# Kernel optimization log

Hardware: AMD Instinct MI355X
Metric: run time of the kernel (lower is better)

## Reference

```python
import jax, jax.numpy as jnp
import numpy as np

B, DIM, DQ, H, W, K = 64, 64, 8, 64, 64, 64


def setup_inputs() -> dict:
    key = jax.random.key(0)
    k1, k2, k3 = jax.random.split(key, 3)
    features = jax.random.normal(k1, (B, DIM, H, W), dtype=jnp.float32)
    query = jax.random.normal(k2, (B, DQ, H, W), dtype=jnp.float32)
    # Ensemble of K 1x1 convs (Conv2d(dim, dim_query, 1, bias=False)) -> [K, DQ, DIM]
    weight = jax.random.normal(k3, (K, DQ, DIM), dtype=jnp.float32) * (1.0 / np.sqrt(DIM))
    return {"features": features, "query": query, "weight": weight}


def reference(features, query, weight):
    # Ensemble of K 1x1 convs: key_values [k, b, dq, h, w]
    key_values = jnp.einsum('bchw,kqc->kbqhw', features, weight)
    b = query.shape[0]
    q_flat = query.reshape(b, -1)                       # [b, D], D = dq*h*w
    kv_flat = key_values.reshape(K, b, -1)              # [k, b, D]
    # torch.cdist(query[b,1,D], kv[b,k,D]) -> euclidean distance [b, k]
    diff = kv_flat - q_flat[None, :, :]                 # [k, b, D]
    distance = jnp.sqrt(jnp.sum(diff * diff, axis=-1)).T  # [b, k]
    codes = jnp.argmax(-distance, axis=-1)              # [b]
    # gather per-batch selected key_values
    sel_key_values = key_values[codes, jnp.arange(b)]   # [b, dq, h, w]
    commit_loss = jnp.mean((sel_key_values - query) ** 2)
    return sel_key_values, codes, commit_loss
```

## Files before the change

### kernel.cpp

```cpp
#include <hip/hip_runtime.h>

#define BQ   64
#define CDIM 64
#define DQN  8
#define HWN  4096
#define KKN  64

typedef float  f32x4  __attribute__((ext_vector_type(4)));
typedef short  short8 __attribute__((ext_vector_type(8)));

__device__ __forceinline__ ushort f2bf(float x) {
  uint u = __float_as_uint(x);
  u += 0x7fffu + ((u >> 16) & 1u);
  return (ushort)(u >> 16);
}
__device__ __forceinline__ float bf2f(ushort h) {
  return __uint_as_float(((uint)h) << 16);
}

__device__ __forceinline__ void cvtStore(ushort* __restrict__ H,
                                         ushort* __restrict__ L,
                                         int uoff, float4 f) {
  ushort4 h = make_ushort4((ushort)(__float_as_uint(f.x) >> 16),
                           (ushort)(__float_as_uint(f.y) >> 16),
                           (ushort)(__float_as_uint(f.z) >> 16),
                           (ushort)(__float_as_uint(f.w) >> 16));
  ushort4 l = make_ushort4(f2bf(f.x - bf2f(h.x)), f2bf(f.y - bf2f(h.y)),
                           f2bf(f.z - bf2f(h.z)), f2bf(f.w - bf2f(h.w)));
  *(ushort4*)(H + uoff) = h;
  *(ushort4*)(L + uoff) = l;
}

__global__ __launch_bounds__(256) void k_gram(const float* __restrict__ feat,
                                              const float* __restrict__ qry,
                                              float* __restrict__ part, int chb) {
  __shared__ ushort ldsH[80 * 128];
  __shared__ ushort ldsL[80 * 128];
  int tid = threadIdx.x;
  int wv = tid >> 6, lane = tid & 63;
  int blk = blockIdx.x;
  int b = blk / chb, cb = blk - b * chb;
  int CH = 4096 / chb;
  int hwBase = cb * CH;
  int nch = 32 / chb;
  const float* fb = feat + (size_t)b * (CDIM * HWN);
  const float* qb = qry + (size_t)b * (DQN * HWN);

  for (int i = tid; i < 8 * 128; i += 256) {
    ldsH[72 * 128 + i] = 0;
    ldsL[72 * 128 + i] = 0;
  }

  int g4 = tid & 31;
  int r8 = tid >> 5;
  const float* base[9];
  int uoffs[9];
  #pragma unroll
  for (int it = 0; it < 9; ++it) {
    int r = it * 8 + r8;
    base[it] = ((r < 64) ? (fb + (size_t)r * HWN)
                         : (qb + (size_t)(r - 64) * HWN)) + g4 * 4;
    uoffs[it] = r * 128 + ((g4 * 4) ^ ((r & 7) << 3));
  }

  int frow = lane & 15;
  int fk = (lane >> 4) * 8;
  f32x4 acc[5] = {};

  {
    float4 cur[9];
    #pragma unroll
    for (int it = 0; it < 9; ++it)
      cur[it] = *(const float4*)(base[it] + hwBase);
    #pragma unroll
    for (int it = 0; it < 9; ++it) cvtStore(ldsH, ldsL, uoffs[it], cur[it]);
  }
  __syncthreads();

  for (int ch = 0; ch < nch; ++ch) {
    float4 nxt[9];
    bool hasNext = (ch + 1 < nch);
    if (hasNext) {
      int hw0 = hwBase + (ch + 1) * 128;
      #pragma unroll
      for (int it = 0; it < 9; ++it)
        nxt[it] = *(const float4*)(base[it] + hw0);
    }
    #pragma unroll
    for (int ks = 0; ks < 4; ++ks) {
      short8 fh[5], fl[5];
      #pragma unroll
      for (int t = 0; t < 5; ++t) {
        int row = t * 16 + frow;
        int uo = row * 128 + ((ks * 32 + fk) ^ ((row & 7) << 3));
        fh[t] = *(const short8*)(ldsH + uo);
        fl[t] = *(const short8*)(ldsL + uo);
      }
      short8 bh, bl;
      switch (wv) {
        case 0:  bh = fh[0]; bl = fl[0]; break;
        case 1:  bh = fh[1]; bl = fl[1]; break;
        case 2:  bh = fh[2]; bl = fl[2]; break;
        default: bh = fh[3]; bl = fl[3]; break;
      }
      #pragma unroll
      for (int t = 0; t < 5; ++t) {
        acc[t] = __builtin_amdgcn_mfma_f32_16x16x32_bf16(fh[t], bh, acc[t], 0, 0, 0);
        acc[t] = __builtin_amdgcn_mfma_f32_16x16x32_bf16(fh[t], bl, acc[t], 0, 0, 0);
        acc[t] = __builtin_amdgcn_mfma_f32_16x16x32_bf16(fl[t], bh, acc[t], 0, 0, 0);
      }
    }
    __syncthreads();
    if (hasNext) {
      #pragma unroll
      for (int it = 0; it < 9; ++it) cvtStore(ldsH, ldsL, uoffs[it], nxt[it]);
      __syncthreads();
    }
  }

  float* op = part + (size_t)blk * 4608 + wv * 16 + (lane & 15);
  int r0 = (lane >> 4) * 4;
  #pragma unroll
  for (int t = 0; t < 5; ++t) {
    #pragma unroll
    for (int r = 0; r < 4; ++r) {
      int row = t * 16 + r0 + r;
      if (row < 72) op[row * 64] = acc[t][r];
    }
  }
}

__global__ __launch_bounds__(256) void k_reduce(const float* __restrict__ part,
                                                float* __restrict__ Sarr,
                                                float* __restrict__ Garr, int chb) {
  int g = blockIdx.x * 256 + threadIdx.x;
  int b = g / 1152;
  int o = (g - b * 1152) * 4;
  f32x4 s = {};
  #pragma unroll 8
  for (int cb = 0; cb < chb; ++cb) {
    f32x4 p = *(const f32x4*)(part + (size_t)(b * chb + cb) * 4608 + o);
    s += p;
  }
  int r = o >> 6, c = o & 63;
  if (r < 64)
    *(f32x4*)(Sarr + b * 4096 + r * 64 + c) = s;
  else
    *(f32x4*)(Garr + b * 512 + (r - 64) * 64 + c) = s;
}

__global__ __launch_bounds__(256) void k_dist(const float* __restrict__ Sarr,
                                              const float* __restrict__ Garr,
                                              const float* __restrict__ wt,
                                              float* __restrict__ dist) {
  __shared__ float wl[4][512];
  int tid = threadIdx.x, wv = tid >> 6, lane = tid & 63;
  int wid = blockIdx.x * 4 + wv;
  int b = wid >> 6, k = wid & 63;
  for (int t = lane; t < 512; t += 64) wl[wv][t] = wt[k * 512 + t];
  __syncthreads();
  const float* Sb = Sarr + b * 4096;
  float v[8] = {};
  #pragma unroll 4
  for (int j = 0; j < 64; ++j) {
    float s = Sb[j * 64 + lane];
    #pragma unroll
    for (int q = 0; q < 8; ++q) v[q] = fmaf(s, wl[wv][q * 64 + j], v[q]);
  }
  double red = 0.0;
  #pragma unroll
  for (int q = 0; q < 8; ++q) {
    float wqi = wl[wv][q * 64 + lane];
    float gqi = Garr[b * 512 + q * 64 + lane];
    red += (double)wqi * ((double)v[q] - 2.0 * (double)gqi);
  }
  #pragma unroll
  for (int off = 32; off; off >>= 1) red += __shfl_xor(red, off);
  if (lane == 0) dist[b * 64 + k] = (float)red;
}

__global__ void k_argmin(const float* __restrict__ dist, int* __restrict__ codes,
                         float* __restrict__ outCodes) {
  int b = blockIdx.x, k = threadIdx.x;
  float d = dist[b * 64 + k];
  int bi = k;
  #pragma unroll
  for (int off = 32; off; off >>= 1) {
    float d2 = __shfl_xor(d, off);
    int i2 = __shfl_xor(bi, off);
    if (d2 < d || (d2 == d && i2 < bi)) { d = d2; bi = i2; }
  }
  if (k == 0) { codes[b] = bi; outCodes[b] = (float)bi; }
}

__global__ __launch_bounds__(256) void k_select(const float* __restrict__ feat,
                                                const float* __restrict__ qry,
                                                const float* __restrict__ wt,
                                                const int* __restrict__ codes,
                                                float* __restrict__ outSel,
                                                float* __restrict__ lossPart) {
  __shared__ float wl[512];
  __shared__ float lred[4];
  int bid = blockIdx.x, tid = threadIdx.x;
  int b = bid >> 2, chunk = bid & 3;
  int code = codes[b];
  wl[tid] = wt[code * 512 + tid];
  wl[tid + 256] = wt[code * 512 + 256 + tid];
  __syncthreads();
  int hw = chunk * 1024 + tid * 4;
  const float* fb = feat + (size_t)b * (CDIM * HWN);
  float4 acc[8] = {};
  #pragma unroll 4
  for (int c = 0; c < 64; ++c) {
    float4 f = *(const float4*)(fb + c * HWN + hw);
    #pragma unroll
    for (int q = 0; q < 8; ++q) {
      float w = wl[q * 64 + c];
      acc[q].x = fmaf(w, f.x, acc[q].x);
      acc[q].y = fmaf(w, f.y, acc[q].y);
      acc[q].z = fmaf(w, f.z, acc[q].z);
      acc[q].w = fmaf(w, f.w, acc[q].w);
    }
  }
  float lsum = 0.f;
  #pragma unroll
  for (int q = 0; q < 8; ++q) {
    size_t off = (size_t)b * 32768 + q * 4096 + hw;
    float4 qv = *(const float4*)(qry + off);
    *(float4*)(outSel + off) = acc[q];
    float dx = acc[q].x - qv.x, dy = acc[q].y - qv.y;
    float dz = acc[q].z - qv.z, dw = acc[q].w - qv.w;
    lsum += dx * dx + dy * dy + dz * dz + dw * dw;
  }
  #pragma unroll
  for (int off = 32; off; off >>= 1) lsum += __shfl_xor(lsum, off);
  if ((tid & 63) == 0) lred[tid >> 6] = lsum;
  __syncthreads();
  if (tid == 0) lossPart[bid] = lred[0] + lred[1] + lred[2] + lred[3];
}

__global__ void k_loss(const float* __restrict__ lossPart, float* __restrict__ outLoss) {
  __shared__ float lred[4];
  int tid = threadIdx.x;
  float s = lossPart[tid];
  #pragma unroll
  for (int off = 32; off; off >>= 1) s += __shfl_xor(s, off);
  if ((tid & 63) == 0) lred[tid >> 6] = s;
  __syncthreads();
  if (tid == 0) outLoss[0] = (lred[0] + lred[1] + lred[2] + lred[3]) * (1.0f / 2097152.0f);
}

extern "C" void kernel_launch(void* const* d_in, const int* in_sizes, int n_in,
                              void* d_out, int out_size, void* d_ws, size_t ws_size,
                              hipStream_t stream) {
  const float* feat = (const float*)d_in[0];
  const float* qry  = (const float*)d_in[1];
  const float* wt   = (const float*)d_in[2];
  float* out = (float*)d_out;
  float* sel      = out;
  float* outCodes = out + 2097152;
  float* outLoss  = out + 2097216;

  int chb = 8;
  while (chb > 1 &&
         ((size_t)64 * chb * 4608 + 64 * 4096 + 64 * 512 + 4096 + 64 + 256) * 4 > ws_size)
    chb >>= 1;
  float* wsf = (float*)d_ws;
  float* part = wsf;
  float* Sarr = part + (size_t)64 * chb * 4608;
  float* Garr = Sarr + 64 * 4096;
  float* dist = Garr + 64 * 512;
  int*   codes = (int*)(dist + 4096);
  float* lossPart = (float*)(codes + 64);

  k_gram<<<64 * chb, 256, 0, stream>>>(feat, qry, part, chb);
  k_reduce<<<(64 * 1152) / 256, 256, 0, stream>>>(part, Sarr, Garr, chb);
  k_dist<<<1024, 256, 0, stream>>>(Sarr, Garr, wt, dist);
  k_argmin<<<64, 64, 0, stream>>>(dist, codes, outCodes);
  k_select<<<256, 256, 0, stream>>>(feat, qry, wt, codes, sel, lossPart);
  k_loss<<<1, 256, 0, stream>>>(lossPart, outLoss);
}
```

Baseline: 59.77 us.

## Drop gram register prefetch, raise occupancy and split count, fuse argmin into select

The gram kernel drops its register double-buffered prefetch in favor of a simple load-convert-store then compute loop, and adds a launch-bounds occupancy hint of 4 blocks. The default HW split per batch goes from 8 to 16 blocks, giving more blocks with shorter loops. The separate argmin kernel is folded into k_select, where each block recomputes the argmin with a wave shuffle and removes one launch. The cost is that global-load latency is no longer hidden behind MFMA work within a block, so the change relies on more resident blocks to cover it, and the larger partial buffer adds reduce traffic.

```diff
diff --git a/kernel.cpp b/kernel.cpp
--- a/kernel.cpp
+++ b/kernel.cpp
@@ -31,9 +31,9 @@
   *(ushort4*)(L + uoff) = l;
 }
 
-__global__ __launch_bounds__(256) void k_gram(const float* __restrict__ feat,
-                                              const float* __restrict__ qry,
-                                              float* __restrict__ part, int chb) {
+__global__ __launch_bounds__(256, 4) void k_gram(const float* __restrict__ feat,
+                                                 const float* __restrict__ qry,
+                                                 float* __restrict__ part, int chb) {
   __shared__ ushort ldsH[80 * 128];
   __shared__ ushort ldsL[80 * 128];
   int tid = threadIdx.x;
@@ -42,7 +42,7 @@
   int b = blk / chb, cb = blk - b * chb;
   int CH = 4096 / chb;
   int hwBase = cb * CH;
-  int nch = 32 / chb;
+  int nch = CH >> 7;
   const float* fb = feat + (size_t)b * (CDIM * HWN);
   const float* qb = qry + (size_t)b * (DQN * HWN);
 
@@ -53,39 +53,22 @@
 
   int g4 = tid & 31;
   int r8 = tid >> 5;
-  const float* base[9];
-  int uoffs[9];
-  #pragma unroll
-  for (int it = 0; it < 9; ++it) {
-    int r = it * 8 + r8;
-    base[it] = ((r < 64) ? (fb + (size_t)r * HWN)
-                         : (qb + (size_t)(r - 64) * HWN)) + g4 * 4;
-    uoffs[it] = r * 128 + ((g4 * 4) ^ ((r & 7) << 3));
-  }
-
   int frow = lane & 15;
   int fk = (lane >> 4) * 8;
   f32x4 acc[5] = {};
 
-  {
-    float4 cur[9];
-    #pragma unroll
-    for (int it = 0; it < 9; ++it)
-      cur[it] = *(const float4*)(base[it] + hwBase);
-    #pragma unroll
-    for (int it = 0; it < 9; ++it) cvtStore(ldsH, ldsL, uoffs[it], cur[it]);
-  }
-  __syncthreads();
-
   for (int ch = 0; ch < nch; ++ch) {
-    float4 nxt[9];
-    bool hasNext = (ch + 1 < nch);
-    if (hasNext) {
-      int hw0 = hwBase + (ch + 1) * 128;
-      #pragma unroll
-      for (int it = 0; it < 9; ++it)
-        nxt[it] = *(const float4*)(base[it] + hw0);
-    }
+    int hw0 = hwBase + ch * 128;
+    #pragma unroll
+    for (int it = 0; it < 9; ++it) {
+      int r = it * 8 + r8;
+      const float* src = (r < 64) ? (fb + (size_t)r * HWN + hw0 + g4 * 4)
+                                  : (qb + (size_t)(r - 64) * HWN + hw0 + g4 * 4);
+      float4 f = *(const float4*)src;
+      int uoff = r * 128 + ((g4 * 4) ^ ((r & 7) << 3));
+      cvtStore(ldsH, ldsL, uoff, f);
+    }
+    __syncthreads();
     #pragma unroll
     for (int ks = 0; ks < 4; ++ks) {
       short8 fh[5], fl[5];
@@ -111,11 +94,6 @@
       }
     }
     __syncthreads();
-    if (hasNext) {
-      #pragma unroll
-      for (int it = 0; it < 9; ++it) cvtStore(ldsH, ldsL, uoffs[it], nxt[it]);
-      __syncthreads();
-    }
   }
 
   float* op = part + (size_t)blk * 4608 + wv * 16 + (lane & 15);
@@ -179,31 +157,29 @@
   if (lane == 0) dist[b * 64 + k] = (float)red;
 }
 
-__global__ void k_argmin(const float* __restrict__ dist, int* __restrict__ codes,
-                         float* __restrict__ outCodes) {
-  int b = blockIdx.x, k = threadIdx.x;
-  float d = dist[b * 64 + k];
-  int bi = k;
+__global__ __launch_bounds__(256) void k_select(const float* __restrict__ feat,
+                                                const float* __restrict__ qry,
+                                                const float* __restrict__ wt,
+                                                const float* __restrict__ dist,
+                                                float* __restrict__ outSel,
+                                                float* __restrict__ outCodes,
+                                                float* __restrict__ lossPart) {
+  __shared__ float wl[512];
+  __shared__ float lred[4];
+  int bid = blockIdx.x, tid = threadIdx.x;
+  int b = bid >> 2, chunk = bid & 2 ? (bid & 3) : (bid & 3);
+  chunk = bid & 3;
+  int lane = tid & 63;
+  float d = dist[b * 64 + lane];
+  int bi = lane;
   #pragma unroll
   for (int off = 32; off; off >>= 1) {
     float d2 = __shfl_xor(d, off);
     int i2 = __shfl_xor(bi, off);
     if (d2 < d || (d2 == d && i2 < bi)) { d = d2; bi = i2; }
   }
-  if (k == 0) { codes[b] = bi; outCodes[b] = (float)bi; }
-}
-
-__global__ __launch_bounds__(256) void k_select(const float* __restrict__ feat,
-                                                const float* __restrict__ qry,
-                                                const float* __restrict__ wt,
-                                                const int* __restrict__ codes,
-                                                float* __restrict__ outSel,
-                                                float* __restrict__ lossPart) {
-  __shared__ float wl[512];
-  __shared__ float lred[4];
-  int bid = blockIdx.x, tid = threadIdx.x;
-  int b = bid >> 2, chunk = bid & 3;
-  int code = codes[b];
+  int code = bi;
+  if (chunk == 0 && tid == 0) outCodes[b] = (float)code;
   wl[tid] = wt[code * 512 + tid];
   wl[tid + 256] = wt[code * 512 + 256 + tid];
   __syncthreads();
@@ -261,22 +237,20 @@
   float* outCodes = out + 2097152;
   float* outLoss  = out + 2097216;
 
-  int chb = 8;
+  int chb = 16;
   while (chb > 1 &&
-         ((size_t)64 * chb * 4608 + 64 * 4096 + 64 * 512 + 4096 + 64 + 256) * 4 > ws_size)
+         ((size_t)64 * chb * 4608 + 64 * 4096 + 64 * 512 + 4096 + 256) * 4 > ws_size)
     chb >>= 1;
   float* wsf = (float*)d_ws;
   float* part = wsf;
   float* Sarr = part + (size_t)64 * chb * 4608;
   float* Garr = Sarr + 64 * 4096;
   float* dist = Garr + 64 * 512;
-  int*   codes = (int*)(dist + 4096);
-  float* lossPart = (float*)(codes + 64);
+  float* lossPart = dist + 4096;
 
   k_gram<<<64 * chb, 256, 0, stream>>>(feat, qry, part, chb);
   k_reduce<<<(64 * 1152) / 256, 256, 0, stream>>>(part, Sarr, Garr, chb);
   k_dist<<<1024, 256, 0, stream>>>(Sarr, Garr, wt, dist);
-  k_argmin<<<64, 64, 0, stream>>>(dist, codes, outCodes);
-  k_select<<<256, 256, 0, stream>>>(feat, qry, wt, codes, sel, lossPart);
+  k_select<<<256, 256, 0, stream>>>(feat, qry, wt, dist, sel, outCodes, lossPart);
   k_loss<<<1, 256, 0, stream>>>(lossPart, outLoss);
 }
```

After: 50.44 us. 1.18x faster.
